# Performance work log

Hardware: AMD Instinct MI355X
Metric: run time of the kernel (lower is better)

Reference implementation:

```python
import jax, jax.numpy as jnp
import numpy as np

N_NODES = 100000
N_EDGES = 600000
HIDDEN = 128
ALPHA = 0.1
K_HOPS = 10


def setup_inputs() -> dict:
    key = jax.random.key(0)
    k1, k2, k3, k4 = jax.random.split(key, 4)
    x = jax.random.normal(k1, (N_NODES, HIDDEN), dtype=jnp.float32)
    edge_index = jax.random.randint(k2, (2, N_EDGES), 0, N_NODES, dtype=jnp.int64)
    W = jax.random.normal(k3, (HIDDEN, HIDDEN), dtype=jnp.float32) * (1.0 / np.sqrt(HIDDEN))
    b = jax.random.normal(k4, (HIDDEN,), dtype=jnp.float32) * 0.01
    return {"x": x, "edge_index": edge_index, "W": W, "b": b}


def reference(x, edge_index, W, b):
    N = x.shape[0]
    # Linear projection (PyTorch convention: y = x W^T + b)
    h = x @ W.T + b

    # gcn_norm with added self-loops (PyG APPNPConv default)
    loop = jnp.arange(N, dtype=edge_index.dtype)
    src = jnp.concatenate([edge_index[0], loop])  # [E+N]
    dst = jnp.concatenate([edge_index[1], loop])
    ones = jnp.ones(src.shape[0], dtype=h.dtype)
    deg = jax.ops.segment_sum(ones, dst, num_segments=N)  # in-degree incl. self-loop
    dinv = jnp.where(deg > 0, jax.lax.rsqrt(deg), 0.0)
    norm = dinv[src] * dinv[dst]  # [E+N]

    # APPNP propagation: h <- (1-alpha) * A_hat h + alpha * h0
    h0 = h
    for _ in range(K_HOPS):
        msg = norm[:, None] * h[src]  # gather + scale
        agg = jax.ops.segment_sum(msg, dst, num_segments=N)  # scatter-add
        h = (1.0 - ALPHA) * agg + ALPHA * h0
    return h
```

## Files before the change

kernel.cpp:

```cpp
#include <hip/hip_runtime.h>

#define N_NODES_C 100000
#define N_EDGES_C 600000
#define HIDDEN_C 128
#define K_HOPS_C 10
#define SCAN_B 98

typedef short short8 __attribute__((ext_vector_type(8)));
typedef float f32x16 __attribute__((ext_vector_type(16)));

__device__ __forceinline__ unsigned short f2bf(float f) {
    unsigned u = __float_as_uint(f);
    return (unsigned short)((u + 0x7FFFu + ((u >> 16) & 1u)) >> 16);
}
__device__ __forceinline__ float bf_lo(unsigned p) { return __uint_as_float(p << 16); }
__device__ __forceinline__ float bf_hi(unsigned p) { return __uint_as_float(p & 0xFFFF0000u); }

__global__ void k_deg(const int* __restrict__ dst, int* __restrict__ deg, int E) {
    int e = blockIdx.x * blockDim.x + threadIdx.x;
    if (e < E) atomicAdd(&deg[dst[e]], 1);
}

__global__ __launch_bounds__(1024) void k_scan_a(const int* __restrict__ deg,
                                                 int* __restrict__ offs,
                                                 int* __restrict__ blksum,
                                                 float* __restrict__ dinv, int N) {
    __shared__ int wtot[16];
    int tid = threadIdx.x;
    int i = blockIdx.x * 1024 + tid;
    int lane = tid & 63;
    int wid = tid >> 6;
    int v = (i < N) ? deg[i] : 0;
    if (i < N) dinv[i] = rsqrtf((float)(v + 1));
    int incl = v;
#pragma unroll
    for (int d = 1; d < 64; d <<= 1) {
        int t = __shfl_up(incl, (unsigned)d, 64);
        if (lane >= d) incl += t;
    }
    if (lane == 63) wtot[wid] = incl;
    __syncthreads();
    int woff = 0, btot = 0;
#pragma unroll
    for (int w = 0; w < 16; ++w) {
        int t = wtot[w];
        if (w < wid) woff += t;
        btot += t;
    }
    if (i < N) offs[i] = woff + incl - v;
    if (tid == 0) blksum[blockIdx.x] = btot;
}

__global__ __launch_bounds__(128) void k_scan_b(const int* __restrict__ blksum,
                                                int* __restrict__ blkoff,
                                                int* __restrict__ offs, int NB, int N) {
    __shared__ int wt[2];
    int t = threadIdx.x;
    int lane = t & 63;
    int w = t >> 6;
    int v = (t < NB) ? blksum[t] : 0;
    int incl = v;
#pragma unroll
    for (int d = 1; d < 64; d <<= 1) {
        int s = __shfl_up(incl, (unsigned)d, 64);
        if (lane >= d) incl += s;
    }
    if (lane == 63) wt[w] = incl;
    __syncthreads();
    int excl = incl - v + (w == 1 ? wt[0] : 0);
    if (t < NB) blkoff[t] = excl;
    if (t == 127) offs[N] = wt[0] + wt[1];
}

__global__ __launch_bounds__(1024) void k_scan_c(int* __restrict__ offs,
                                                 int* __restrict__ cursor,
                                                 const int* __restrict__ blkoff, int N) {
    int i = blockIdx.x * 1024 + threadIdx.x;
    if (i < N) {
        int v = offs[i] + blkoff[blockIdx.x];
        offs[i] = v;
        cursor[i] = v;
    }
}

__global__ void k_fill(const int* __restrict__ src, const int* __restrict__ dst,
                       const float* __restrict__ dinv, int* __restrict__ cursor,
                       uint2* __restrict__ csr, int E) {
    int e = blockIdx.x * blockDim.x + threadIdx.x;
    if (e < E) {
        int s = src[e], d = dst[e];
        int pos = atomicAdd(&cursor[d], 1);
        uint2 v;
        v.x = (unsigned)s;
        v.y = __float_as_uint(dinv[s] * dinv[d]);
        csr[pos] = v;
    }
}

__global__ __launch_bounds__(256) void k_gemm(const float* __restrict__ x,
                                              const float* __restrict__ W,
                                              const float* __restrict__ b,
                                              unsigned short* __restrict__ hb, int N) {
    __shared__ unsigned short Wb[HIDDEN_C * HIDDEN_C];
    int tid = threadIdx.x;
#pragma unroll
    for (int i = 0; i < 8; ++i) {
        int c = tid + 256 * i;
        int m = c >> 4;
        int g = c & 15;
        const float4* wsrc = (const float4*)W + m * 32 + g * 2;
        float4 wa = wsrc[0];
        float4 wb = wsrc[1];
        unsigned short t8[8];
        t8[0] = f2bf(wa.x); t8[1] = f2bf(wa.y); t8[2] = f2bf(wa.z); t8[3] = f2bf(wa.w);
        t8[4] = f2bf(wb.x); t8[5] = f2bf(wb.y); t8[6] = f2bf(wb.z); t8[7] = f2bf(wb.w);
        int gs = g ^ (m & 15);
        *(uint4*)&Wb[m * 128 + gs * 8] = *(const uint4*)t8;
    }
    __syncthreads();

    int lane = tid & 63;
    int wv = tid >> 6;
    int row0 = blockIdx.x * 128 + wv * 32;
    int m = lane & 31;
    int half = lane >> 5;

    int row = row0 + m;
    if (row >= N) row = N - 1;
    const float4* xrow = (const float4*)(x + (size_t)row * 128);

    f32x16 acc[4];
#pragma unroll
    for (int t = 0; t < 4; ++t)
#pragma unroll
        for (int r = 0; r < 16; ++r) acc[t][r] = 0.f;

    for (int s = 0; s < 8; ++s) {
        int kb = s * 16 + half * 8;
        float4 x0 = xrow[kb >> 2];
        float4 x1 = xrow[(kb >> 2) + 1];
        union { unsigned short u[8]; short8 v; } af;
        af.u[0] = f2bf(x0.x); af.u[1] = f2bf(x0.y); af.u[2] = f2bf(x0.z); af.u[3] = f2bf(x0.w);
        af.u[4] = f2bf(x1.x); af.u[5] = f2bf(x1.y); af.u[6] = f2bf(x1.z); af.u[7] = f2bf(x1.w);
        int g = kb >> 3;
#pragma unroll
        for (int t = 0; t < 4; ++t) {
            int r = t * 32 + m;
            short8 bfrag = *(const short8*)&Wb[r * 128 + ((g ^ (r & 15)) << 3)];
            acc[t] = __builtin_amdgcn_mfma_f32_32x32x16_bf16(af.v, bfrag, acc[t], 0, 0, 0);
        }
    }

    float bias[4];
#pragma unroll
    for (int t = 0; t < 4; ++t) bias[t] = b[t * 32 + m];
#pragma unroll
    for (int t = 0; t < 4; ++t) {
#pragma unroll
        for (int r = 0; r < 16; ++r) {
            int rrow = (r & 3) + 8 * (r >> 2) + 4 * half;
            int node = row0 + rrow;
            if (node < N) {
                float v = acc[t][r] + bias[t];
                hb[(size_t)node * 128 + t * 32 + m] = f2bf(v);
            }
        }
    }
}

__global__ __launch_bounds__(256) void k_prop(const uint4* __restrict__ hin4,
                                              const uint4* __restrict__ h04,
                                              uint4* __restrict__ hout_b,
                                              float* __restrict__ hout_f,
                                              const int* __restrict__ offs,
                                              const uint2* __restrict__ csr,
                                              const float* __restrict__ dinv,
                                              int N, int final_hop) {
    int tid = threadIdx.x;
    int lane = tid & 63;
    int wid = tid >> 6;
    int q = lane >> 4;
    int f = lane & 15;

    int node = (blockIdx.x * 4 + wid) * 4 + q;
    bool valid = node < N;

    int beg = 0, end = 0;
    if (valid) {
        beg = offs[node];
        end = offs[node + 1];
    }

    uint4 hq = make_uint4(0u, 0u, 0u, 0u);
    uint4 ps = make_uint4(0u, 0u, 0u, 0u);
    float ws = 0.f;
    if (valid) {
        hq = h04[(size_t)node * 16 + f];
        ps = hin4[(size_t)node * 16 + f];
        float dv = dinv[node];
        ws = dv * dv;
    }

    float acc[8];
#pragma unroll
    for (int i = 0; i < 8; ++i) acc[i] = 0.f;

    int j = beg;
#pragma unroll 2
    for (; j + 2 <= end; j += 2) {
        uint2 e0 = csr[j];
        uint2 e1 = csr[j + 1];
        uint4 p0 = hin4[(size_t)e0.x * 16 + f];
        uint4 p1 = hin4[(size_t)e1.x * 16 + f];
        float w0 = __uint_as_float(e0.y);
        float w1 = __uint_as_float(e1.y);
        acc[0] += w0 * bf_lo(p0.x); acc[1] += w0 * bf_hi(p0.x);
        acc[2] += w0 * bf_lo(p0.y); acc[3] += w0 * bf_hi(p0.y);
        acc[4] += w0 * bf_lo(p0.z); acc[5] += w0 * bf_hi(p0.z);
        acc[6] += w0 * bf_lo(p0.w); acc[7] += w0 * bf_hi(p0.w);
        acc[0] += w1 * bf_lo(p1.x); acc[1] += w1 * bf_hi(p1.x);
        acc[2] += w1 * bf_lo(p1.y); acc[3] += w1 * bf_hi(p1.y);
        acc[4] += w1 * bf_lo(p1.z); acc[5] += w1 * bf_hi(p1.z);
        acc[6] += w1 * bf_lo(p1.w); acc[7] += w1 * bf_hi(p1.w);
    }
    if (j < end) {
        uint2 e = csr[j];
        uint4 p = hin4[(size_t)e.x * 16 + f];
        float w = __uint_as_float(e.y);
        acc[0] += w * bf_lo(p.x); acc[1] += w * bf_hi(p.x);
        acc[2] += w * bf_lo(p.y); acc[3] += w * bf_hi(p.y);
        acc[4] += w * bf_lo(p.z); acc[5] += w * bf_hi(p.z);
        acc[6] += w * bf_lo(p.w); acc[7] += w * bf_hi(p.w);
    }

    acc[0] += ws * bf_lo(ps.x); acc[1] += ws * bf_hi(ps.x);
    acc[2] += ws * bf_lo(ps.y); acc[3] += ws * bf_hi(ps.y);
    acc[4] += ws * bf_lo(ps.z); acc[5] += ws * bf_hi(ps.z);
    acc[6] += ws * bf_lo(ps.w); acc[7] += ws * bf_hi(ps.w);

    if (valid) {
        float o[8];
        o[0] = 0.9f * acc[0] + 0.1f * bf_lo(hq.x);
        o[1] = 0.9f * acc[1] + 0.1f * bf_hi(hq.x);
        o[2] = 0.9f * acc[2] + 0.1f * bf_lo(hq.y);
        o[3] = 0.9f * acc[3] + 0.1f * bf_hi(hq.y);
        o[4] = 0.9f * acc[4] + 0.1f * bf_lo(hq.z);
        o[5] = 0.9f * acc[5] + 0.1f * bf_hi(hq.z);
        o[6] = 0.9f * acc[6] + 0.1f * bf_lo(hq.w);
        o[7] = 0.9f * acc[7] + 0.1f * bf_hi(hq.w);
        if (final_hop) {
            float4* dst0 = (float4*)(hout_f + (size_t)node * 128 + f * 8);
            float4 v0; v0.x = o[0]; v0.y = o[1]; v0.z = o[2]; v0.w = o[3];
            float4 v1; v1.x = o[4]; v1.y = o[5]; v1.z = o[6]; v1.w = o[7];
            dst0[0] = v0;
            dst0[1] = v1;
        } else {
            uint4 p;
            p.x = (unsigned)f2bf(o[0]) | ((unsigned)f2bf(o[1]) << 16);
            p.y = (unsigned)f2bf(o[2]) | ((unsigned)f2bf(o[3]) << 16);
            p.z = (unsigned)f2bf(o[4]) | ((unsigned)f2bf(o[5]) << 16);
            p.w = (unsigned)f2bf(o[6]) | ((unsigned)f2bf(o[7]) << 16);
            hout_b[(size_t)node * 16 + f] = p;
        }
    }
}

extern "C" void kernel_launch(void* const* d_in, const int* in_sizes, int n_in,
                              void* d_out, int out_size, void* d_ws, size_t ws_size,
                              hipStream_t stream) {
    const float* x = (const float*)d_in[0];
    const int* edge = (const int*)d_in[1];
    const float* W = (const float*)d_in[2];
    const float* b = (const float*)d_in[3];
    float* out = (float*)d_out;

    const int N = N_NODES_C;
    const int E = N_EDGES_C;
    const int* src = edge;
    const int* dst = edge + E;

    char* ws = (char*)d_ws;
    size_t off = 0;
    auto carve = [&](size_t bytes) -> void* {
        void* p = ws + off;
        off = (off + bytes + 511) & ~(size_t)511;
        return p;
    };
    unsigned short* h0b = (unsigned short*)carve((size_t)N * HIDDEN_C * 2);
    unsigned short* bA  = (unsigned short*)carve((size_t)N * HIDDEN_C * 2);
    unsigned short* bB  = (unsigned short*)carve((size_t)N * HIDDEN_C * 2);
    int*   deg     = (int*)  carve((size_t)N * sizeof(int));
    float* dinv    = (float*)carve((size_t)N * sizeof(float));
    int*   offs    = (int*)  carve((size_t)(N + 1) * sizeof(int));
    int*   cursor  = (int*)  carve((size_t)N * sizeof(int));
    uint2* csr     = (uint2*)carve((size_t)E * sizeof(uint2));
    int*   blksum  = (int*)  carve((size_t)SCAN_B * sizeof(int));
    int*   blkoff  = (int*)  carve((size_t)SCAN_B * sizeof(int));
    (void)ws_size;

    hipMemsetAsync(deg, 0, (size_t)N * sizeof(int), stream);

    int eb = (E + 255) / 256;
    k_deg<<<eb, 256, 0, stream>>>(dst, deg, E);
    k_scan_a<<<SCAN_B, 1024, 0, stream>>>(deg, offs, blksum, dinv, N);
    k_scan_b<<<1, 128, 0, stream>>>(blksum, blkoff, offs, SCAN_B, N);
    k_scan_c<<<SCAN_B, 1024, 0, stream>>>(offs, cursor, blkoff, N);
    k_fill<<<eb, 256, 0, stream>>>(src, dst, dinv, cursor, csr, E);

    k_gemm<<<(N + 127) / 128, 256, 0, stream>>>(x, W, b, h0b, N);

    const uint4* hin = (const uint4*)h0b;
    for (int k = 0; k < K_HOPS_C; ++k) {
        int fin = (k == K_HOPS_C - 1);
        uint4* houtb = ((k & 1) == 0) ? (uint4*)bA : (uint4*)bB;
        k_prop<<<(N + 15) / 16, 256, 0, stream>>>(hin, (const uint4*)h0b,
                                                  fin ? nullptr : houtb,
                                                  fin ? out : nullptr,
                                                  offs, csr, dinv, N, fin);
        hin = houtb;
    }
}
```

Before: 509.8 us.

## Bucket nodes by in-degree so propagation wavefronts process similar-degree nodes

Builds a histogram of node in-degrees (capped at 63), scans it into bucket offsets, and writes a degree-sorted permutation of nodes with packed begin/end CSR ranges. The propagation kernel now maps each 16-lane group to a permuted slot, so the four nodes in a wavefront have similar edge counts and less divergence in the edge loop. The cost is heavy atomic contention on 64 bucket counters during setup, an extra indirection per node, and scattered node-row reads and writes that lose spatial locality.

```diff
diff --git a/kernel.cpp b/kernel.cpp
--- a/kernel.cpp
+++ b/kernel.cpp
@@ -24,14 +24,18 @@
 __global__ __launch_bounds__(1024) void k_scan_a(const int* __restrict__ deg,
                                                  int* __restrict__ offs,
                                                  int* __restrict__ blksum,
-                                                 float* __restrict__ dinv, int N) {
+                                                 float* __restrict__ dinv,
+                                                 int* __restrict__ deghist, int N) {
     __shared__ int wtot[16];
     int tid = threadIdx.x;
     int i = blockIdx.x * 1024 + tid;
     int lane = tid & 63;
     int wid = tid >> 6;
     int v = (i < N) ? deg[i] : 0;
-    if (i < N) dinv[i] = rsqrtf((float)(v + 1));
+    if (i < N) {
+        dinv[i] = rsqrtf((float)(v + 1));
+        atomicAdd(&deghist[v < 63 ? v : 63], 1);
+    }
     int incl = v;
 #pragma unroll
     for (int d = 1; d < 64; d <<= 1) {
@@ -53,7 +57,10 @@
 
 __global__ __launch_bounds__(128) void k_scan_b(const int* __restrict__ blksum,
                                                 int* __restrict__ blkoff,
-                                                int* __restrict__ offs, int NB, int N) {
+                                                int* __restrict__ offs,
+                                                const int* __restrict__ deghist,
+                                                int* __restrict__ bucketcur,
+                                                int NB, int N) {
     __shared__ int wt[2];
     int t = threadIdx.x;
     int lane = t & 63;
@@ -70,16 +77,34 @@
     int excl = incl - v + (w == 1 ? wt[0] : 0);
     if (t < NB) blkoff[t] = excl;
     if (t == 127) offs[N] = wt[0] + wt[1];
+    if (w == 0) {
+        int hv = deghist[lane];
+        int hincl = hv;
+#pragma unroll
+        for (int d = 1; d < 64; d <<= 1) {
+            int s = __shfl_up(hincl, (unsigned)d, 64);
+            if (lane >= d) hincl += s;
+        }
+        bucketcur[lane] = hincl - hv;
+    }
 }
 
 __global__ __launch_bounds__(1024) void k_scan_c(int* __restrict__ offs,
                                                  int* __restrict__ cursor,
-                                                 const int* __restrict__ blkoff, int N) {
+                                                 const int* __restrict__ blkoff,
+                                                 const int* __restrict__ deg,
+                                                 int* __restrict__ bucketcur,
+                                                 int* __restrict__ perm,
+                                                 uint2* __restrict__ begend, int N) {
     int i = blockIdx.x * 1024 + threadIdx.x;
     if (i < N) {
         int v = offs[i] + blkoff[blockIdx.x];
         offs[i] = v;
         cursor[i] = v;
+        int d = deg[i];
+        int pos = atomicAdd(&bucketcur[d < 63 ? d : 63], 1);
+        perm[pos] = i;
+        begend[pos] = make_uint2((unsigned)v, (unsigned)(v + d));
     }
 }
 
@@ -172,7 +197,8 @@
                                               const uint4* __restrict__ h04,
                                               uint4* __restrict__ hout_b,
                                               float* __restrict__ hout_f,
-                                              const int* __restrict__ offs,
+                                              const int* __restrict__ perm,
+                                              const uint2* __restrict__ begend,
                                               const uint2* __restrict__ csr,
                                               const float* __restrict__ dinv,
                                               int N, int final_hop) {
@@ -182,13 +208,15 @@
     int q = lane >> 4;
     int f = lane & 15;
 
-    int node = (blockIdx.x * 4 + wid) * 4 + q;
-    bool valid = node < N;
-
-    int beg = 0, end = 0;
+    int slot = (blockIdx.x * 4 + wid) * 4 + q;
+    bool valid = slot < N;
+
+    int node = 0, beg = 0, end = 0;
     if (valid) {
-        beg = offs[node];
-        end = offs[node + 1];
+        node = perm[slot];
+        uint2 be = begend[slot];
+        beg = (int)be.x;
+        end = (int)be.y;
     }
 
     uint4 hq = make_uint4(0u, 0u, 0u, 0u);
@@ -289,22 +317,26 @@
     unsigned short* h0b = (unsigned short*)carve((size_t)N * HIDDEN_C * 2);
     unsigned short* bA  = (unsigned short*)carve((size_t)N * HIDDEN_C * 2);
     unsigned short* bB  = (unsigned short*)carve((size_t)N * HIDDEN_C * 2);
-    int*   deg     = (int*)  carve((size_t)N * sizeof(int));
+    int*   deg     = (int*)  carve(((size_t)N + 64) * sizeof(int));
+    int*   deghist = deg + N;
     float* dinv    = (float*)carve((size_t)N * sizeof(float));
     int*   offs    = (int*)  carve((size_t)(N + 1) * sizeof(int));
     int*   cursor  = (int*)  carve((size_t)N * sizeof(int));
     uint2* csr     = (uint2*)carve((size_t)E * sizeof(uint2));
     int*   blksum  = (int*)  carve((size_t)SCAN_B * sizeof(int));
     int*   blkoff  = (int*)  carve((size_t)SCAN_B * sizeof(int));
+    int*   bucketcur = (int*)carve(64 * sizeof(int));
+    int*   perm    = (int*)  carve((size_t)N * sizeof(int));
+    uint2* begend  = (uint2*)carve((size_t)N * sizeof(uint2));
     (void)ws_size;
 
-    hipMemsetAsync(deg, 0, (size_t)N * sizeof(int), stream);
+    hipMemsetAsync(deg, 0, ((size_t)N + 64) * sizeof(int), stream);
 
     int eb = (E + 255) / 256;
     k_deg<<<eb, 256, 0, stream>>>(dst, deg, E);
-    k_scan_a<<<SCAN_B, 1024, 0, stream>>>(deg, offs, blksum, dinv, N);
-    k_scan_b<<<1, 128, 0, stream>>>(blksum, blkoff, offs, SCAN_B, N);
-    k_scan_c<<<SCAN_B, 1024, 0, stream>>>(offs, cursor, blkoff, N);
+    k_scan_a<<<SCAN_B, 1024, 0, stream>>>(deg, offs, blksum, dinv, deghist, N);
+    k_scan_b<<<1, 128, 0, stream>>>(blksum, blkoff, offs, deghist, bucketcur, SCAN_B, N);
+    k_scan_c<<<SCAN_B, 1024, 0, stream>>>(offs, cursor, blkoff, deg, bucketcur, perm, begend, N);
     k_fill<<<eb, 256, 0, stream>>>(src, dst, dinv, cursor, csr, E);
 
     k_gemm<<<(N + 127) / 128, 256, 0, stream>>>(x, W, b, h0b, N);
@@ -316,7 +348,7 @@
         k_prop<<<(N + 15) / 16, 256, 0, stream>>>(hin, (const uint4*)h0b,
                                                   fin ? nullptr : houtb,
                                                   fin ? out : nullptr,
-                                                  offs, csr, dinv, N, fin);
+                                                  perm, begend, csr, dinv, N, fin);
         hin = houtb;
     }
 }
```

After: 1.259 ms. +147.0%, slower.
